# Kernel optimization log

Hardware: AMD Instinct MI355X
Metric: run time of the kernel (lower is better)

## Reference

```python
import jax, jax.numpy as jnp
import numpy as np

EPS = 1e-6  # torch.nn.PairwiseDistance default eps, added elementwise before the norm


def setup_inputs() -> dict:
    key = jax.random.key(0)
    k1, k2 = jax.random.split(key)
    source_prompt = jax.random.normal(k1, (50, 768), dtype=jnp.float32)      # [P, D]
    patch_embeds = jax.random.normal(k2, (1024, 197, 768), dtype=jnp.float32)  # [N, M, D]
    return {"source_prompt": source_prompt, "patch_embeds": patch_embeds, "src_task": 0}


def reference(source_prompt, patch_embeds, src_task):
    # torch: for each patch_embed [M,D], PairwiseDistance(src[:,None,:], pe[None,:,:])
    #   = ||src - pe + eps||_2 over last dim -> [P, M]; accumulate .mean(); divide by N.
    # lax.scan over N keeps peak memory at one [P, M, D] diff tensor, matching the
    # sequential reduction of the original loop without Python-level iteration.
    def step(acc, pe):                      # pe: [M, D]
        diff = source_prompt[:, None, :] - pe[None, :, :] + EPS   # [P, M, D]
        d = jnp.sqrt(jnp.sum(diff * diff, axis=-1))               # [P, M]
        return acc + jnp.mean(d), None

    total, _ = jax.lax.scan(step, jnp.zeros((), dtype=source_prompt.dtype), patch_embeds)
    return total / patch_embeds.shape[0]
```

## Files before the change

### kernel.cpp

```cpp
#include <hip/hip_runtime.h>


typedef __attribute__((ext_vector_type(8))) short bf16x8;
typedef __attribute__((ext_vector_type(4))) float f32x4;

#define D_DIM 768
#define NM_TOTAL 201728
#define COLS_PER_WG 128
#define NUM_WG (NM_TOTAL / COLS_PER_WG)
#define KC 64
#define NCHUNK (D_DIM / KC)

__device__ __forceinline__ unsigned short f2bf(float f) {
  unsigned int u = __float_as_uint(f);
  u += 0x7FFFu + ((u >> 16) & 1u);
  return (unsigned short)(u >> 16);
}

__global__ void prep_kernel(const float* __restrict__ src,
                            short* __restrict__ aW,
                            float* __restrict__ na) {
  const int r = blockIdx.x;
  const int lane = threadIdx.x;
  float sq = 0.f;
#pragma unroll
  for (int j = 0; j < 12; ++j) {
    const int c = lane + j * 64;
    float v = 0.f;
    if (r < 50) v = src[r * D_DIM + c] + 1e-6f;
    sq += v * v;
    aW[r * D_DIM + c] = (short)f2bf(v);
  }
#pragma unroll
  for (int m = 32; m >= 1; m >>= 1) sq += __shfl_xor(sq, m);
  if (lane == 0) na[r] = sq;
}

__global__ __launch_bounds__(512, 4) void dist_kernel(
    const float* __restrict__ pe,
    const short* __restrict__ aW,
    const float* __restrict__ na,
    float* __restrict__ partials) {
  __shared__ __attribute__((aligned(16))) float buf[2][COLS_PER_WG * KC];

  const int tid  = threadIdx.x;
  const int wave = tid >> 6;
  const int lane = tid & 63;
  const int quad = lane >> 4;
  const int l16  = lane & 15;
  const int colL = wave * 16 + l16;
  const int col0 = blockIdx.x * COLS_PER_WG;

  const int s_sub = lane >> 4;
  const int cpos  = lane & 15;

  const short* a0p = aW + (size_t)(0 * 16 + l16) * D_DIM;
  const short* a1p = aW + (size_t)(1 * 16 + l16) * D_DIM;
  const short* a2p = aW + (size_t)(2 * 16 + l16) * D_DIM;
  const short* a3p = aW + (size_t)(3 * 16 + l16) * D_DIM;

  f32x4 acc0 = {0.f, 0.f, 0.f, 0.f};
  f32x4 acc1 = {0.f, 0.f, 0.f, 0.f};
  f32x4 acc2 = {0.f, 0.f, 0.f, 0.f};
  f32x4 acc3 = {0.f, 0.f, 0.f, 0.f};
  float nb = 0.f;

#pragma unroll
  for (int r = 0; r < 4; ++r) {
    const int cl   = wave * 16 + r * 4 + s_sub;
    const int cdat = cpos ^ (cl & 15);
    const float* g = pe + (size_t)(col0 + cl) * D_DIM + cdat * 4;
    __builtin_amdgcn_global_load_lds(
        (const __attribute__((address_space(1))) void*)g,
        (__attribute__((address_space(3))) void*)&buf[0][(wave * 16 + r * 4) * KC],
        16, 0, 0);
  }
  __syncthreads();

  for (int it = 0; it < NCHUNK; ++it) {
    const int cur = it & 1;
    if (it + 1 < NCHUNK) {
#pragma unroll
      for (int r = 0; r < 4; ++r) {
        const int cl   = wave * 16 + r * 4 + s_sub;
        const int cdat = cpos ^ (cl & 15);
        const float* g = pe + (size_t)(col0 + cl) * D_DIM + (it + 1) * KC + cdat * 4;
        __builtin_amdgcn_global_load_lds(
            (const __attribute__((address_space(1))) void*)g,
            (__attribute__((address_space(3))) void*)&buf[cur ^ 1][(wave * 16 + r * 4) * KC],
            16, 0, 0);
      }
    }

    const float* bufc = buf[cur];
#pragma unroll
    for (int s = 0; s < 2; ++s) {
      const int kbase = it * KC + s * 32;
      const int P0 = s * 8 + quad * 2;
      const f32x4 u0 = *(const f32x4*)&bufc[colL * KC + ((P0 ^ l16) << 2)];
      const f32x4 u1 = *(const f32x4*)&bufc[colL * KC + (((P0 + 1) ^ l16) << 2)];

      nb = fmaf(u0.x, u0.x, nb); nb = fmaf(u0.y, u0.y, nb);
      nb = fmaf(u0.z, u0.z, nb); nb = fmaf(u0.w, u0.w, nb);
      nb = fmaf(u1.x, u1.x, nb); nb = fmaf(u1.y, u1.y, nb);
      nb = fmaf(u1.z, u1.z, nb); nb = fmaf(u1.w, u1.w, nb);

      union { bf16x8 v; unsigned short u[8]; } b;
      b.u[0] = f2bf(u0.x); b.u[1] = f2bf(u0.y);
      b.u[2] = f2bf(u0.z); b.u[3] = f2bf(u0.w);
      b.u[4] = f2bf(u1.x); b.u[5] = f2bf(u1.y);
      b.u[6] = f2bf(u1.z); b.u[7] = f2bf(u1.w);

      bf16x8 af0 = *(const bf16x8*)(a0p + kbase + quad * 8);
      bf16x8 af1 = *(const bf16x8*)(a1p + kbase + quad * 8);
      bf16x8 af2 = *(const bf16x8*)(a2p + kbase + quad * 8);
      bf16x8 af3 = *(const bf16x8*)(a3p + kbase + quad * 8);

      acc0 = __builtin_amdgcn_mfma_f32_16x16x32_bf16(af0, b.v, acc0, 0, 0, 0);
      acc1 = __builtin_amdgcn_mfma_f32_16x16x32_bf16(af1, b.v, acc1, 0, 0, 0);
      acc2 = __builtin_amdgcn_mfma_f32_16x16x32_bf16(af2, b.v, acc2, 0, 0, 0);
      acc3 = __builtin_amdgcn_mfma_f32_16x16x32_bf16(af3, b.v, acc3, 0, 0, 0);
    }
    __syncthreads();
  }

  nb += __shfl_xor(nb, 16);
  nb += __shfl_xor(nb, 32);

  float s = 0.f;
  {
    f32x4 accs[4] = {acc0, acc1, acc2, acc3};
#pragma unroll
    for (int t = 0; t < 4; ++t) {
#pragma unroll
      for (int r = 0; r < 4; ++r) {
        const int p = t * 16 + quad * 4 + r;
        if (p < 50) {
          const float c = accs[t][r];
          const float d2 = fmaxf(na[p] + nb - 2.f * c, 0.f);
          s += sqrtf(d2);
        }
      }
    }
  }

#pragma unroll
  for (int m = 32; m >= 1; m >>= 1) s += __shfl_xor(s, m);

  float* wsum = (float*)buf;
  if (lane == 0) wsum[wave] = s;
  __syncthreads();
  if (tid == 0) {
    float t = 0.f;
#pragma unroll
    for (int i = 0; i < 8; ++i) t += wsum[i];
    partials[blockIdx.x] = t;
  }
}

__global__ void finalize_kernel(const float* __restrict__ partials,
                                float* __restrict__ out) {
  __shared__ float red[256];
  float s = 0.f;
  for (int i = threadIdx.x; i < NUM_WG; i += 256) s += partials[i];
  red[threadIdx.x] = s;
  __syncthreads();
  for (int step = 128; step >= 1; step >>= 1) {
    if (threadIdx.x < step) red[threadIdx.x] += red[threadIdx.x + step];
    __syncthreads();
  }
  if (threadIdx.x == 0) out[0] = red[0] * (1.0f / 10086400.0f);
}

extern "C" void kernel_launch(void* const* d_in, const int* in_sizes, int n_in,
                              void* d_out, int out_size, void* d_ws, size_t ws_size,
                              hipStream_t stream) {
  const float* src = (const float*)d_in[0];
  const float* pe  = (const float*)d_in[1];
  float* out = (float*)d_out;

  char* ws = (char*)d_ws;
  float* partials = (float*)ws;
  float* na       = (float*)(ws + 8192);
  short* aW       = (short*)(ws + 16384);

  prep_kernel<<<64, 64, 0, stream>>>(src, aW, na);
  dist_kernel<<<NUM_WG, 512, 0, stream>>>(pe, aW, na, partials);
  finalize_kernel<<<1, 256, 0, stream>>>(partials, out);
}
```

Baseline: 843.6 us.

## Make LDS staging wave-private and replace block barriers with vmcnt waits

Result: no change. 841.3 us (-0.3%).

```diff
diff --git a/kernel.cpp b/kernel.cpp
--- a/kernel.cpp
+++ b/kernel.cpp
@@ -10,6 +10,7 @@
 #define NUM_WG (NM_TOTAL / COLS_PER_WG)
 #define KC 64
 #define NCHUNK (D_DIM / KC)
+#define CPW 16
 
 __device__ __forceinline__ unsigned short f2bf(float f) {
   unsigned int u = __float_as_uint(f);
@@ -41,23 +42,18 @@
     const short* __restrict__ aW,
     const float* __restrict__ na,
     float* __restrict__ partials) {
-  __shared__ __attribute__((aligned(16))) float buf[2][COLS_PER_WG * KC];
+  __shared__ __attribute__((aligned(16))) float buf[8][2][CPW * KC];
 
   const int tid  = threadIdx.x;
   const int wave = tid >> 6;
   const int lane = tid & 63;
   const int quad = lane >> 4;
   const int l16  = lane & 15;
-  const int colL = wave * 16 + l16;
-  const int col0 = blockIdx.x * COLS_PER_WG;
+
+  const int colbase = blockIdx.x * COLS_PER_WG + wave * CPW;
 
   const int s_sub = lane >> 4;
   const int cpos  = lane & 15;
-
-  const short* a0p = aW + (size_t)(0 * 16 + l16) * D_DIM;
-  const short* a1p = aW + (size_t)(1 * 16 + l16) * D_DIM;
-  const short* a2p = aW + (size_t)(2 * 16 + l16) * D_DIM;
-  const short* a3p = aW + (size_t)(3 * 16 + l16) * D_DIM;
 
   f32x4 acc0 = {0.f, 0.f, 0.f, 0.f};
   f32x4 acc1 = {0.f, 0.f, 0.f, 0.f};
@@ -67,38 +63,47 @@
 
 #pragma unroll
   for (int r = 0; r < 4; ++r) {
-    const int cl   = wave * 16 + r * 4 + s_sub;
-    const int cdat = cpos ^ (cl & 15);
-    const float* g = pe + (size_t)(col0 + cl) * D_DIM + cdat * 4;
+    const int cl = r * 4 + s_sub;
+    const float* g = pe + (size_t)(colbase + cl) * D_DIM + ((cpos ^ cl) << 2);
     __builtin_amdgcn_global_load_lds(
         (const __attribute__((address_space(1))) void*)g,
-        (__attribute__((address_space(3))) void*)&buf[0][(wave * 16 + r * 4) * KC],
+        (__attribute__((address_space(3))) void*)&buf[wave][0][(r * 4) * KC],
         16, 0, 0);
   }
-  __syncthreads();
 
   for (int it = 0; it < NCHUNK; ++it) {
     const int cur = it & 1;
+
+    bf16x8 af[2][4];
+#pragma unroll
+    for (int s = 0; s < 2; ++s)
+#pragma unroll
+      for (int t = 0; t < 4; ++t)
+        af[s][t] = *(const bf16x8*)(aW + (size_t)(t * 16 + l16) * D_DIM +
+                                    it * KC + s * 32 + quad * 8);
+
     if (it + 1 < NCHUNK) {
 #pragma unroll
       for (int r = 0; r < 4; ++r) {
-        const int cl   = wave * 16 + r * 4 + s_sub;
-        const int cdat = cpos ^ (cl & 15);
-        const float* g = pe + (size_t)(col0 + cl) * D_DIM + (it + 1) * KC + cdat * 4;
+        const int cl = r * 4 + s_sub;
+        const float* g = pe + (size_t)(colbase + cl) * D_DIM + (it + 1) * KC +
+                         ((cpos ^ cl) << 2);
         __builtin_amdgcn_global_load_lds(
             (const __attribute__((address_space(1))) void*)g,
-            (__attribute__((address_space(3))) void*)&buf[cur ^ 1][(wave * 16 + r * 4) * KC],
+            (__attribute__((address_space(3))) void*)&buf[wave][cur ^ 1][(r * 4) * KC],
             16, 0, 0);
       }
+      asm volatile("s_waitcnt vmcnt(4)" ::: "memory");
+    } else {
+      asm volatile("s_waitcnt vmcnt(0)" ::: "memory");
     }
 
-    const float* bufc = buf[cur];
+    const float* bufc = buf[wave][cur];
 #pragma unroll
     for (int s = 0; s < 2; ++s) {
-      const int kbase = it * KC + s * 32;
       const int P0 = s * 8 + quad * 2;
-      const f32x4 u0 = *(const f32x4*)&bufc[colL * KC + ((P0 ^ l16) << 2)];
-      const f32x4 u1 = *(const f32x4*)&bufc[colL * KC + (((P0 + 1) ^ l16) << 2)];
+      const f32x4 u0 = *(const f32x4*)&bufc[l16 * KC + ((P0 ^ l16) << 2)];
+      const f32x4 u1 = *(const f32x4*)&bufc[l16 * KC + (((P0 + 1) ^ l16) << 2)];
 
       nb = fmaf(u0.x, u0.x, nb); nb = fmaf(u0.y, u0.y, nb);
       nb = fmaf(u0.z, u0.z, nb); nb = fmaf(u0.w, u0.w, nb);
@@ -111,17 +116,11 @@
       b.u[4] = f2bf(u1.x); b.u[5] = f2bf(u1.y);
       b.u[6] = f2bf(u1.z); b.u[7] = f2bf(u1.w);
 
-      bf16x8 af0 = *(const bf16x8*)(a0p + kbase + quad * 8);
-      bf16x8 af1 = *(const bf16x8*)(a1p + kbase + quad * 8);
-      bf16x8 af2 = *(const bf16x8*)(a2p + kbase + quad * 8);
-      bf16x8 af3 = *(const bf16x8*)(a3p + kbase + quad * 8);
-
-      acc0 = __builtin_amdgcn_mfma_f32_16x16x32_bf16(af0, b.v, acc0, 0, 0, 0);
-      acc1 = __builtin_amdgcn_mfma_f32_16x16x32_bf16(af1, b.v, acc1, 0, 0, 0);
-      acc2 = __builtin_amdgcn_mfma_f32_16x16x32_bf16(af2, b.v, acc2, 0, 0, 0);
-      acc3 = __builtin_amdgcn_mfma_f32_16x16x32_bf16(af3, b.v, acc3, 0, 0, 0);
+      acc0 = __builtin_amdgcn_mfma_f32_16x16x32_bf16(af[s][0], b.v, acc0, 0, 0, 0);
+      acc1 = __builtin_amdgcn_mfma_f32_16x16x32_bf16(af[s][1], b.v, acc1, 0, 0, 0);
+      acc2 = __builtin_amdgcn_mfma_f32_16x16x32_bf16(af[s][2], b.v, acc2, 0, 0, 0);
+      acc3 = __builtin_amdgcn_mfma_f32_16x16x32_bf16(af[s][3], b.v, acc3, 0, 0, 0);
     }
-    __syncthreads();
   }
 
   nb += __shfl_xor(nb, 16);
@@ -147,6 +146,7 @@
 #pragma unroll
   for (int m = 32; m >= 1; m >>= 1) s += __shfl_xor(s, m);
 
+  __syncthreads();
   float* wsum = (float*)buf;
   if (lane == 0) wsum[wave] = s;
   __syncthreads();
```
